# Kernel tuning notes

Hardware: AMD Instinct MI355X
Metric: run time of the kernel (lower is better)

## Reference

```python
import jax, jax.numpy as jnp
import numpy as np

HIDDEN_DIM = 128
ATTN_DIM = 64
B, N = 2, 512

def setup_inputs() -> dict:
    key = jax.random.key(0)
    ks = jax.random.split(key, 8)
    s = 0.05
    return {
        "X":    jax.random.normal(ks[0], (B, N, HIDDEN_DIM), dtype=jnp.float32),
        "Wo":   jax.random.normal(ks[1], (ATTN_DIM, HIDDEN_DIM), dtype=jnp.float32) * s,
        "W1":   jax.random.normal(ks[2], (ATTN_DIM, HIDDEN_DIM), dtype=jnp.float32) * s,
        "Wphi": jax.random.normal(ks[3], (ATTN_DIM,), dtype=jnp.float32) * s,
        "Wy":   jax.random.normal(ks[4], (HIDDEN_DIM, HIDDEN_DIM), dtype=jnp.float32) * s,
        "by":   jax.random.normal(ks[5], (HIDDEN_DIM,), dtype=jnp.float32) * s,
        "We":   jax.random.normal(ks[6], (HIDDEN_DIM, ATTN_DIM), dtype=jnp.float32) * s,
        "be":   jax.random.normal(ks[7], (HIDDEN_DIM,), dtype=jnp.float32) * s,
    }

def reference(X, Wo, W1, Wphi, Wy, by, We, be):
    # h_o, h_1: [B, N, A]
    h_o = jnp.einsum('bnc,ac->bna', X, Wo)
    h_1 = jnp.einsum('bnc,ac->bna', X, W1)
    # pairwise tanh edge features e_ij: [B, N, N, A]
    e = jnp.tanh(h_o[:, :, None, :] + h_1[:, None, :, :])
    # scores [B, N, N] via w_phi projection, row-wise softmax over j
    scores = jnp.einsum('bija,a->bij', e, Wphi)
    alpha = jax.nn.softmax(scores, axis=-1)
    # value path 1: Wy x_j -> aggregated by alpha (bmm)
    X_y = jnp.einsum('bnc,hc->bnh', X, Wy) + by
    part1 = jnp.einsum('bij,bjh->bih', alpha, X_y)
    # value path 2: We e_ij -> weighted sum over j
    eval_ = jnp.einsum('bija,ha->bijh', e, We) + be  # [B, N, N, H]
    part2 = jnp.einsum('bij,bijh->bih', alpha, eval_)
    return part1 + part2
```

## Files before the change

kernel.cpp:

```cpp
#include <hip/hip_runtime.h>

#define B_ 2
#define N_ 512
#define C_ 128
#define A_ 64
#define H_ 128

#define SC2L 2.885390081777927f
#define NEG2LE -2.885390081777927f

#define OFF_V   0
#define OFF_UT8 (OFF_V   + B_*N_*A_)
#define OFF_US8 (OFF_UT8 + B_*N_*A_/2)
#define OFF_XYP (OFF_US8 + B_*N_*A_/2)

#define WES_STRIDE 130

__device__ __forceinline__ float fexp2(float x) { return __builtin_amdgcn_exp2f(x); }
__device__ __forceinline__ float frcp(float x)  { return __builtin_amdgcn_rcpf(x); }
__device__ __forceinline__ unsigned f2bf(float x) {
  unsigned u = __float_as_uint(x);
  return (u + 0x7fffu + ((u >> 16) & 1u)) >> 16;
}
__device__ __forceinline__ float bf_lo(unsigned d) { return __uint_as_float(d << 16); }
__device__ __forceinline__ float bf_hi(unsigned d) { return __uint_as_float(d & 0xffff0000u); }

__global__ __launch_bounds__(256) void proj_kernel(
    const float* __restrict__ X, const float* __restrict__ by,
    const float* __restrict__ Wo, const float* __restrict__ W1,
    const float* __restrict__ Wy, float* __restrict__ ws) {
  __shared__ float xs[2*C_];
  int row0 = blockIdx.x * 2;
  int t = threadIdx.x;
  if (t < 2*C_) xs[t] = X[(size_t)row0*C_ + t];
  __syncthreads();

  const float* wrow;
  int col;
  if (t < 64)       { col = t;       wrow = Wo + (size_t)col*C_; }
  else if (t < 128) { col = t - 64;  wrow = W1 + (size_t)col*C_; }
  else              { col = t - 128; wrow = Wy + (size_t)col*C_; }

  const float4* w4 = (const float4*)wrow;
  float acc0 = 0.f, acc1 = 0.f;
  #pragma unroll 8
  for (int c4 = 0; c4 < C_/4; ++c4) {
    float4 w = w4[c4];
    int c = c4*4;
    acc0 = fmaf(xs[c+0], w.x, acc0);  acc1 = fmaf(xs[C_+c+0], w.x, acc1);
    acc0 = fmaf(xs[c+1], w.y, acc0);  acc1 = fmaf(xs[C_+c+1], w.y, acc1);
    acc0 = fmaf(xs[c+2], w.z, acc0);  acc1 = fmaf(xs[C_+c+2], w.z, acc1);
    acc0 = fmaf(xs[c+3], w.w, acc0);  acc1 = fmaf(xs[C_+c+3], w.w, acc1);
  }

  int b = row0 >> 9, n0 = row0 & (N_-1);

  if (t < 64) {
    float* o = ws + OFF_V + (size_t)row0*A_ + col;
    o[0] = fexp2(SC2L * acc0);
    o[A_] = fexp2(SC2L * acc1);
  } else if (t < 128) {
    int a = col;
    unsigned u0 = f2bf(fexp2(SC2L * acc0));
    unsigned u1 = f2bf(fexp2(SC2L * acc1));
    unsigned short* ut = (unsigned short*)(ws + OFF_UT8);
    size_t bA = ((size_t)(b*8 + (a >> 3))*N_ + n0)*8 + (a & 7);
    ut[bA] = (unsigned short)u0;
    ut[bA + 8] = (unsigned short)u1;
    unsigned short* us = (unsigned short*)(ws + OFF_US8);
    size_t bC = ((size_t)(b*64 + (n0 >> 3))*A_ + a)*8 + (n0 & 7);
    us[bC] = (unsigned short)u0;
    us[bC + 1] = (unsigned short)u1;
  } else {
    int h = col;
    float bb = by[h];
    unsigned xv0 = f2bf(acc0 + bb);
    unsigned xv1 = f2bf(acc1 + bb);
    unsigned* xp = (unsigned*)(ws + OFF_XYP);
    xp[(size_t)(b*(N_/2) + (n0 >> 1))*H_ + h] = xv0 | (xv1 << 16);
  }
}

__global__ __launch_bounds__(1024) void attn_kernel(
    const float* __restrict__ Wphi, const float* __restrict__ be,
    const float* __restrict__ We,
    const float* __restrict__ ws, float* __restrict__ out) {
  __shared__ __align__(16) float pkv[2][A_];
  __shared__ __align__(16) float pkw[A_];
  __shared__ float sc[2][N_];
  __shared__ float reds[16];
  __shared__ float ebw[2][16][A_];
  __shared__ float ebar[2][A_];
  __shared__ __align__(16) float p1s[2][32][H_];
  __shared__ float wes[A_*WES_STRIDE];

  int t = threadIdx.x;
  int w = t >> 6, lane = t & 63;
  int blk = blockIdx.x;
  int b = blk >> 8;
  int i0 = (blk & 255) * 2;
  int g0 = b*N_ + i0;

  const uint4* ut8 = (const uint4*)((const unsigned short*)(ws + OFF_UT8))
                     + (size_t)b*8*N_;
  const uint4* us8 = (const uint4*)((const unsigned short*)(ws + OFF_US8))
                     + (size_t)b*64*A_;
  const uint4* xy4 = (const uint4*)((const unsigned*)(ws + OFF_XYP))
                     + (size_t)b*(N_/2)*(H_/4);

  if (t < 2*A_) {
    int r = t >> 6, a = t & 63;
    pkv[r][a] = ws[OFF_V + (size_t)(g0 + r)*A_ + a];
  } else if (t < 3*A_) {
    pkw[t - 2*A_] = Wphi[t - 2*A_];
  }
  #pragma unroll
  for (int e = t; e < H_*A_; e += 1024) {
    int h = e >> 6, a = e & 63;
    wes[a*WES_STRIDE + h] = We[e];
  }
  __syncthreads();

  {
    int r = t >> 9, j = t & 511;
    const float4* pv4 = (const float4*)pkv[r];
    const float4* pw4 = (const float4*)pkw;
    float s = 0.f;
    #pragma unroll
    for (int g = 0; g < 8; ++g) {
      uint4 d = ut8[(size_t)g*N_ + j];
      float4 v0 = pv4[2*g], v1 = pv4[2*g + 1];
      float4 w0 = pw4[2*g], w1 = pw4[2*g + 1];
      s = fmaf(w0.x, frcp(fmaf(v0.x, bf_lo(d.x), 1.f)), s);
      s = fmaf(w0.y, frcp(fmaf(v0.y, bf_hi(d.x), 1.f)), s);
      s = fmaf(w0.z, frcp(fmaf(v0.z, bf_lo(d.y), 1.f)), s);
      s = fmaf(w0.w, frcp(fmaf(v0.w, bf_hi(d.y), 1.f)), s);
      s = fmaf(w1.x, frcp(fmaf(v1.x, bf_lo(d.z), 1.f)), s);
      s = fmaf(w1.y, frcp(fmaf(v1.y, bf_hi(d.z), 1.f)), s);
      s = fmaf(w1.z, frcp(fmaf(v1.z, bf_lo(d.w), 1.f)), s);
      s = fmaf(w1.w, frcp(fmaf(v1.w, bf_hi(d.w), 1.f)), s);
    }
    float p = fexp2(NEG2LE * s);
    sc[r][j] = p;
    float q = p;
    #pragma unroll
    for (int m = 1; m < 64; m <<= 1) q += __shfl_xor(q, m);
    if (lane == 0) reds[w] = q;
  }
  __syncthreads();

  {
    float v0 = pkv[0][lane], v1 = pkv[1][lane];
    const float4* s40 = (const float4*)sc[0];
    const float4* s41 = (const float4*)sc[1];
    float c0 = 0.f, c1 = 0.f;
    #pragma unroll
    for (int oo = 0; oo < 4; ++oo) {
      int o = oo*16 + w;
      uint4 d = us8[(size_t)o*A_ + lane];
      float u0 = bf_lo(d.x), u1 = bf_hi(d.x), u2 = bf_lo(d.y), u3 = bf_hi(d.y);
      float u4 = bf_lo(d.z), u5 = bf_hi(d.z), u6 = bf_lo(d.w), u7 = bf_hi(d.w);
      float4 pA0 = s40[o*2], pB0 = s40[o*2 + 1];
      float4 pA1 = s41[o*2], pB1 = s41[o*2 + 1];
      float r0 = frcp(fmaf(v0, u0, 1.f)), q0 = frcp(fmaf(v1, u0, 1.f));
      float r1 = frcp(fmaf(v0, u1, 1.f)), q1 = frcp(fmaf(v1, u1, 1.f));
      float r2 = frcp(fmaf(v0, u2, 1.f)), q2 = frcp(fmaf(v1, u2, 1.f));
      float r3 = frcp(fmaf(v0, u3, 1.f)), q3 = frcp(fmaf(v1, u3, 1.f));
      float r4 = frcp(fmaf(v0, u4, 1.f)), q4 = frcp(fmaf(v1, u4, 1.f));
      float r5 = frcp(fmaf(v0, u5, 1.f)), q5 = frcp(fmaf(v1, u5, 1.f));
      float r6 = frcp(fmaf(v0, u6, 1.f)), q6 = frcp(fmaf(v1, u6, 1.f));
      float r7 = frcp(fmaf(v0, u7, 1.f)), q7 = frcp(fmaf(v1, u7, 1.f));
      c0 = fmaf(pA0.x, r0, c0); c1 = fmaf(pA1.x, q0, c1);
      c0 = fmaf(pA0.y, r1, c0); c1 = fmaf(pA1.y, q1, c1);
      c0 = fmaf(pA0.z, r2, c0); c1 = fmaf(pA1.z, q2, c1);
      c0 = fmaf(pA0.w, r3, c0); c1 = fmaf(pA1.w, q3, c1);
      c0 = fmaf(pB0.x, r4, c0); c1 = fmaf(pB1.x, q4, c1);
      c0 = fmaf(pB0.y, r5, c0); c1 = fmaf(pB1.y, q5, c1);
      c0 = fmaf(pB0.z, r6, c0); c1 = fmaf(pB1.z, q6, c1);
      c0 = fmaf(pB0.w, r7, c0); c1 = fmaf(pB1.w, q7, c1);
    }
    ebw[0][w][lane] = c0;
    ebw[1][w][lane] = c1;
  }

  {
    int h4 = t & 31, qd = t >> 5;
    float d0 = 0.f, d1 = 0.f, d2 = 0.f, d3 = 0.f;
    float e0 = 0.f, e1 = 0.f, e2 = 0.f, e3 = 0.f;
    const float2* p20 = (const float2*)sc[0];
    const float2* p21 = (const float2*)sc[1];
    #pragma unroll
    for (int kc = 0; kc < 8; ++kc) {
      int k = qd*8 + kc;
      uint4 d = xy4[(size_t)k*(H_/4) + h4];
      float2 P0 = p20[k];
      float2 P1 = p21[k];
      float xa = bf_lo(d.x), xb = bf_hi(d.x);
      float xc = bf_lo(d.y), xd = bf_hi(d.y);
      float xe = bf_lo(d.z), xf = bf_hi(d.z);
      float xg = bf_lo(d.w), xh = bf_hi(d.w);
      d0 = fmaf(P0.x, xa, d0); d0 = fmaf(P0.y, xb, d0);
      d1 = fmaf(P0.x, xc, d1); d1 = fmaf(P0.y, xd, d1);
      d2 = fmaf(P0.x, xe, d2); d2 = fmaf(P0.y, xf, d2);
      d3 = fmaf(P0.x, xg, d3); d3 = fmaf(P0.y, xh, d3);
      e0 = fmaf(P1.x, xa, e0); e0 = fmaf(P1.y, xb, e0);
      e1 = fmaf(P1.x, xc, e1); e1 = fmaf(P1.y, xd, e1);
      e2 = fmaf(P1.x, xe, e2); e2 = fmaf(P1.y, xf, e2);
      e3 = fmaf(P1.x, xg, e3); e3 = fmaf(P1.y, xh, e3);
    }
    *(float4*)&p1s[0][qd][h4*4] = make_float4(d0, d1, d2, d3);
    *(float4*)&p1s[1][qd][h4*4] = make_float4(e0, e1, e2, e3);
  }
  __syncthreads();

  if (t < 2*A_) {
    int r = t >> 6, a = t & 63;
    float e = 0.f;
    #pragma unroll
    for (int k = 0; k < 16; ++k) e += ebw[r][k][a];
    float l = 0.f;
    #pragma unroll
    for (int k = 0; k < 8; ++k) l += reds[r*8 + k];
    ebar[r][a] = l - 2.0f*e;
  }
  __syncthreads();

  if (t < 2*H_) {
    int r = t >> 7, h = t & 127;
    float l = 0.f;
    #pragma unroll
    for (int k = 0; k < 8; ++k) l += reds[r*8 + k];
    float acc = 0.f;
    #pragma unroll
    for (int k = 0; k < 32; ++k) acc += p1s[r][k][h];
    float e2 = 0.f;
    #pragma unroll 8
    for (int a = 0; a < A_; ++a) e2 = fmaf(ebar[r][a], wes[a*WES_STRIDE + h], e2);
    out[(size_t)(g0 + r)*H_ + h] = (acc + e2) * frcp(l) + be[h];
  }
}

extern "C" void kernel_launch(void* const* d_in, const int* in_sizes, int n_in,
                              void* d_out, int out_size, void* d_ws, size_t ws_size,
                              hipStream_t stream) {
  const float* X    = (const float*)d_in[0];
  const float* Wo   = (const float*)d_in[1];
  const float* W1   = (const float*)d_in[2];
  const float* Wphi = (const float*)d_in[3];
  const float* Wy   = (const float*)d_in[4];
  const float* by   = (const float*)d_in[5];
  const float* We   = (const float*)d_in[6];
  const float* be   = (const float*)d_in[7];
  float* out = (float*)d_out;
  float* ws  = (float*)d_ws;

  hipLaunchKernelGGL(proj_kernel, dim3(B_*N_/2), dim3(256), 0, stream,
                     X, by, Wo, W1, Wy, ws);
  hipLaunchKernelGGL(attn_kernel, dim3(B_*N_/2), dim3(1024), 0, stream,
                     Wphi, be, We, ws, out);
}
```

Measured before the change: 92.50 us.

## Process four query rows per attention block to reuse key-side loads

Each attention block now handles four query rows instead of two, halving the grid to 256 blocks. Each key-side value loaded from global memory (ut8, us8, xy4) and the staged We matrix is reused across twice as many rows, which cuts global traffic and the per-block We staging cost. In exchange, register pressure and shared memory per block go up, and with fewer blocks the 256 CUs of the MI355X get only about one block each, lowering occupancy and latency hiding.

```diff
diff --git a/kernel.cpp b/kernel.cpp
--- a/kernel.cpp
+++ b/kernel.cpp
@@ -85,20 +85,20 @@
     const float* __restrict__ Wphi, const float* __restrict__ be,
     const float* __restrict__ We,
     const float* __restrict__ ws, float* __restrict__ out) {
-  __shared__ __align__(16) float pkv[2][A_];
+  __shared__ __align__(16) float pkv[4][A_];
   __shared__ __align__(16) float pkw[A_];
-  __shared__ float sc[2][N_];
-  __shared__ float reds[16];
-  __shared__ float ebw[2][16][A_];
-  __shared__ float ebar[2][A_];
-  __shared__ __align__(16) float p1s[2][32][H_];
+  __shared__ float sc[4][N_];
+  __shared__ float reds[4][8];
+  __shared__ float ebw[4][16][A_];
+  __shared__ float ebar[4][A_];
+  __shared__ __align__(16) float p1s[4][32][H_];
   __shared__ float wes[A_*WES_STRIDE];
 
   int t = threadIdx.x;
   int w = t >> 6, lane = t & 63;
   int blk = blockIdx.x;
-  int b = blk >> 8;
-  int i0 = (blk & 255) * 2;
+  int b = blk >> 7;
+  int i0 = (blk & 127) * 4;
   int g0 = b*N_ + i0;
 
   const uint4* ut8 = (const uint4*)((const unsigned short*)(ws + OFF_UT8))
@@ -108,11 +108,11 @@
   const uint4* xy4 = (const uint4*)((const unsigned*)(ws + OFF_XYP))
                      + (size_t)b*(N_/2)*(H_/4);
 
-  if (t < 2*A_) {
+  if (t < 4*A_) {
     int r = t >> 6, a = t & 63;
     pkv[r][a] = ws[OFF_V + (size_t)(g0 + r)*A_ + a];
-  } else if (t < 3*A_) {
-    pkw[t - 2*A_] = Wphi[t - 2*A_];
+  } else if (t < 5*A_) {
+    pkw[t - 4*A_] = Wphi[t - 4*A_];
   }
   #pragma unroll
   for (int e = t; e < H_*A_; e += 1024) {
@@ -122,38 +122,61 @@
   __syncthreads();
 
   {
-    int r = t >> 9, j = t & 511;
-    const float4* pv4 = (const float4*)pkv[r];
+    int r2 = t >> 9, j = t & 511;
+    const float4* pvA = (const float4*)pkv[r2];
+    const float4* pvB = (const float4*)pkv[r2 + 2];
     const float4* pw4 = (const float4*)pkw;
-    float s = 0.f;
+    float sA = 0.f, sB = 0.f;
     #pragma unroll
     for (int g = 0; g < 8; ++g) {
       uint4 d = ut8[(size_t)g*N_ + j];
-      float4 v0 = pv4[2*g], v1 = pv4[2*g + 1];
+      float4 a0 = pvA[2*g], a1 = pvA[2*g + 1];
+      float4 b0 = pvB[2*g], b1 = pvB[2*g + 1];
       float4 w0 = pw4[2*g], w1 = pw4[2*g + 1];
-      s = fmaf(w0.x, frcp(fmaf(v0.x, bf_lo(d.x), 1.f)), s);
-      s = fmaf(w0.y, frcp(fmaf(v0.y, bf_hi(d.x), 1.f)), s);
-      s = fmaf(w0.z, frcp(fmaf(v0.z, bf_lo(d.y), 1.f)), s);
-      s = fmaf(w0.w, frcp(fmaf(v0.w, bf_hi(d.y), 1.f)), s);
-      s = fmaf(w1.x, frcp(fmaf(v1.x, bf_lo(d.z), 1.f)), s);
-      s = fmaf(w1.y, frcp(fmaf(v1.y, bf_hi(d.z), 1.f)), s);
-      s = fmaf(w1.z, frcp(fmaf(v1.z, bf_lo(d.w), 1.f)), s);
-      s = fmaf(w1.w, frcp(fmaf(v1.w, bf_hi(d.w), 1.f)), s);
-    }
-    float p = fexp2(NEG2LE * s);
-    sc[r][j] = p;
-    float q = p;
-    #pragma unroll
-    for (int m = 1; m < 64; m <<= 1) q += __shfl_xor(q, m);
-    if (lane == 0) reds[w] = q;
+      float u0 = bf_lo(d.x), u1 = bf_hi(d.x), u2 = bf_lo(d.y), u3 = bf_hi(d.y);
+      float u4 = bf_lo(d.z), u5 = bf_hi(d.z), u6 = bf_lo(d.w), u7 = bf_hi(d.w);
+      sA = fmaf(w0.x, frcp(fmaf(a0.x, u0, 1.f)), sA);
+      sB = fmaf(w0.x, frcp(fmaf(b0.x, u0, 1.f)), sB);
+      sA = fmaf(w0.y, frcp(fmaf(a0.y, u1, 1.f)), sA);
+      sB = fmaf(w0.y, frcp(fmaf(b0.y, u1, 1.f)), sB);
+      sA = fmaf(w0.z, frcp(fmaf(a0.z, u2, 1.f)), sA);
+      sB = fmaf(w0.z, frcp(fmaf(b0.z, u2, 1.f)), sB);
+      sA = fmaf(w0.w, frcp(fmaf(a0.w, u3, 1.f)), sA);
+      sB = fmaf(w0.w, frcp(fmaf(b0.w, u3, 1.f)), sB);
+      sA = fmaf(w1.x, frcp(fmaf(a1.x, u4, 1.f)), sA);
+      sB = fmaf(w1.x, frcp(fmaf(b1.x, u4, 1.f)), sB);
+      sA = fmaf(w1.y, frcp(fmaf(a1.y, u5, 1.f)), sA);
+      sB = fmaf(w1.y, frcp(fmaf(b1.y, u5, 1.f)), sB);
+      sA = fmaf(w1.z, frcp(fmaf(a1.z, u6, 1.f)), sA);
+      sB = fmaf(w1.z, frcp(fmaf(b1.z, u6, 1.f)), sB);
+      sA = fmaf(w1.w, frcp(fmaf(a1.w, u7, 1.f)), sA);
+      sB = fmaf(w1.w, frcp(fmaf(b1.w, u7, 1.f)), sB);
+    }
+    float pA = fexp2(NEG2LE * sA);
+    float pB = fexp2(NEG2LE * sB);
+    sc[r2][j] = pA;
+    sc[r2 + 2][j] = pB;
+    float qA = pA, qB = pB;
+    #pragma unroll
+    for (int m = 1; m < 64; m <<= 1) {
+      qA += __shfl_xor(qA, m);
+      qB += __shfl_xor(qB, m);
+    }
+    if (lane == 0) {
+      reds[r2][w & 7] = qA;
+      reds[r2 + 2][w & 7] = qB;
+    }
   }
   __syncthreads();
 
   {
     float v0 = pkv[0][lane], v1 = pkv[1][lane];
+    float v2 = pkv[2][lane], v3 = pkv[3][lane];
     const float4* s40 = (const float4*)sc[0];
     const float4* s41 = (const float4*)sc[1];
-    float c0 = 0.f, c1 = 0.f;
+    const float4* s42 = (const float4*)sc[2];
+    const float4* s43 = (const float4*)sc[3];
+    float c0 = 0.f, c1 = 0.f, c2 = 0.f, c3 = 0.f;
     #pragma unroll
     for (int oo = 0; oo < 4; ++oo) {
       int o = oo*16 + w;
@@ -162,74 +185,93 @@
       float u4 = bf_lo(d.z), u5 = bf_hi(d.z), u6 = bf_lo(d.w), u7 = bf_hi(d.w);
       float4 pA0 = s40[o*2], pB0 = s40[o*2 + 1];
       float4 pA1 = s41[o*2], pB1 = s41[o*2 + 1];
-      float r0 = frcp(fmaf(v0, u0, 1.f)), q0 = frcp(fmaf(v1, u0, 1.f));
-      float r1 = frcp(fmaf(v0, u1, 1.f)), q1 = frcp(fmaf(v1, u1, 1.f));
-      float r2 = frcp(fmaf(v0, u2, 1.f)), q2 = frcp(fmaf(v1, u2, 1.f));
-      float r3 = frcp(fmaf(v0, u3, 1.f)), q3 = frcp(fmaf(v1, u3, 1.f));
-      float r4 = frcp(fmaf(v0, u4, 1.f)), q4 = frcp(fmaf(v1, u4, 1.f));
-      float r5 = frcp(fmaf(v0, u5, 1.f)), q5 = frcp(fmaf(v1, u5, 1.f));
-      float r6 = frcp(fmaf(v0, u6, 1.f)), q6 = frcp(fmaf(v1, u6, 1.f));
-      float r7 = frcp(fmaf(v0, u7, 1.f)), q7 = frcp(fmaf(v1, u7, 1.f));
-      c0 = fmaf(pA0.x, r0, c0); c1 = fmaf(pA1.x, q0, c1);
-      c0 = fmaf(pA0.y, r1, c0); c1 = fmaf(pA1.y, q1, c1);
-      c0 = fmaf(pA0.z, r2, c0); c1 = fmaf(pA1.z, q2, c1);
-      c0 = fmaf(pA0.w, r3, c0); c1 = fmaf(pA1.w, q3, c1);
-      c0 = fmaf(pB0.x, r4, c0); c1 = fmaf(pB1.x, q4, c1);
-      c0 = fmaf(pB0.y, r5, c0); c1 = fmaf(pB1.y, q5, c1);
-      c0 = fmaf(pB0.z, r6, c0); c1 = fmaf(pB1.z, q6, c1);
-      c0 = fmaf(pB0.w, r7, c0); c1 = fmaf(pB1.w, q7, c1);
+      float4 pA2 = s42[o*2], pB2 = s42[o*2 + 1];
+      float4 pA3 = s43[o*2], pB3 = s43[o*2 + 1];
+      #define PC_STEP(UU, F) { \
+        float r0 = frcp(fmaf(v0, UU, 1.f)); \
+        float r1 = frcp(fmaf(v1, UU, 1.f)); \
+        float r2v = frcp(fmaf(v2, UU, 1.f)); \
+        float r3v = frcp(fmaf(v3, UU, 1.f)); \
+        c0 = fmaf(pA0.F, r0, c0); c1 = fmaf(pA1.F, r1, c1); \
+        c2 = fmaf(pA2.F, r2v, c2); c3 = fmaf(pA3.F, r3v, c3); }
+      #define PC_STEP2(UU, F) { \
+        float r0 = frcp(fmaf(v0, UU, 1.f)); \
+        float r1 = frcp(fmaf(v1, UU, 1.f)); \
+        float r2v = frcp(fmaf(v2, UU, 1.f)); \
+        float r3v = frcp(fmaf(v3, UU, 1.f)); \
+        c0 = fmaf(pB0.F, r0, c0); c1 = fmaf(pB1.F, r1, c1); \
+        c2 = fmaf(pB2.F, r2v, c2); c3 = fmaf(pB3.F, r3v, c3); }
+      PC_STEP(u0, x) PC_STEP(u1, y) PC_STEP(u2, z) PC_STEP(u3, w)
+      PC_STEP2(u4, x) PC_STEP2(u5, y) PC_STEP2(u6, z) PC_STEP2(u7, w)
+      #undef PC_STEP
+      #undef PC_STEP2
     }
     ebw[0][w][lane] = c0;
     ebw[1][w][lane] = c1;
+    ebw[2][w][lane] = c2;
+    ebw[3][w][lane] = c3;
   }
 
   {
     int h4 = t & 31, qd = t >> 5;
-    float d0 = 0.f, d1 = 0.f, d2 = 0.f, d3 = 0.f;
-    float e0 = 0.f, e1 = 0.f, e2 = 0.f, e3 = 0.f;
+    float s00=0.f,s01=0.f,s02=0.f,s03=0.f;
+    float s10=0.f,s11=0.f,s12=0.f,s13=0.f;
+    float s20=0.f,s21=0.f,s22=0.f,s23=0.f;
+    float s30=0.f,s31=0.f,s32=0.f,s33=0.f;
     const float2* p20 = (const float2*)sc[0];
     const float2* p21 = (const float2*)sc[1];
+    const float2* p22 = (const float2*)sc[2];
+    const float2* p23 = (const float2*)sc[3];
     #pragma unroll
     for (int kc = 0; kc < 8; ++kc) {
       int k = qd*8 + kc;
       uint4 d = xy4[(size_t)k*(H_/4) + h4];
-      float2 P0 = p20[k];
-      float2 P1 = p21[k];
+      float2 P0 = p20[k], P1 = p21[k], P2 = p22[k], P3 = p23[k];
       float xa = bf_lo(d.x), xb = bf_hi(d.x);
       float xc = bf_lo(d.y), xd = bf_hi(d.y);
       float xe = bf_lo(d.z), xf = bf_hi(d.z);
       float xg = bf_lo(d.w), xh = bf_hi(d.w);
-      d0 = fmaf(P0.x, xa, d0); d0 = fmaf(P0.y, xb, d0);
-      d1 = fmaf(P0.x, xc, d1); d1 = fmaf(P0.y, xd, d1);
-      d2 = fmaf(P0.x, xe, d2); d2 = fmaf(P0.y, xf, d2);
-      d3 = fmaf(P0.x, xg, d3); d3 = fmaf(P0.y, xh, d3);
-      e0 = fmaf(P1.x, xa, e0); e0 = fmaf(P1.y, xb, e0);
-      e1 = fmaf(P1.x, xc, e1); e1 = fmaf(P1.y, xd, e1);
-      e2 = fmaf(P1.x, xe, e2); e2 = fmaf(P1.y, xf, e2);
-      e3 = fmaf(P1.x, xg, e3); e3 = fmaf(P1.y, xh, e3);
-    }
-    *(float4*)&p1s[0][qd][h4*4] = make_float4(d0, d1, d2, d3);
-    *(float4*)&p1s[1][qd][h4*4] = make_float4(e0, e1, e2, e3);
-  }
-  __syncthreads();
-
-  if (t < 2*A_) {
+      s00 = fmaf(P0.x, xa, s00); s00 = fmaf(P0.y, xb, s00);
+      s01 = fmaf(P0.x, xc, s01); s01 = fmaf(P0.y, xd, s01);
+      s02 = fmaf(P0.x, xe, s02); s02 = fmaf(P0.y, xf, s02);
+      s03 = fmaf(P0.x, xg, s03); s03 = fmaf(P0.y, xh, s03);
+      s10 = fmaf(P1.x, xa, s10); s10 = fmaf(P1.y, xb, s10);
+      s11 = fmaf(P1.x, xc, s11); s11 = fmaf(P1.y, xd, s11);
+      s12 = fmaf(P1.x, xe, s12); s12 = fmaf(P1.y, xf, s12);
+      s13 = fmaf(P1.x, xg, s13); s13 = fmaf(P1.y, xh, s13);
+      s20 = fmaf(P2.x, xa, s20); s20 = fmaf(P2.y, xb, s20);
+      s21 = fmaf(P2.x, xc, s21); s21 = fmaf(P2.y, xd, s21);
+      s22 = fmaf(P2.x, xe, s22); s22 = fmaf(P2.y, xf, s22);
+      s23 = fmaf(P2.x, xg, s23); s23 = fmaf(P2.y, xh, s23);
+      s30 = fmaf(P3.x, xa, s30); s30 = fmaf(P3.y, xb, s30);
+      s31 = fmaf(P3.x, xc, s31); s31 = fmaf(P3.y, xd, s31);
+      s32 = fmaf(P3.x, xe, s32); s32 = fmaf(P3.y, xf, s32);
+      s33 = fmaf(P3.x, xg, s33); s33 = fmaf(P3.y, xh, s33);
+    }
+    *(float4*)&p1s[0][qd][h4*4] = make_float4(s00, s01, s02, s03);
+    *(float4*)&p1s[1][qd][h4*4] = make_float4(s10, s11, s12, s13);
+    *(float4*)&p1s[2][qd][h4*4] = make_float4(s20, s21, s22, s23);
+    *(float4*)&p1s[3][qd][h4*4] = make_float4(s30, s31, s32, s33);
+  }
+  __syncthreads();
+
+  if (t < 4*A_) {
     int r = t >> 6, a = t & 63;
     float e = 0.f;
     #pragma unroll
     for (int k = 0; k < 16; ++k) e += ebw[r][k][a];
     float l = 0.f;
     #pragma unroll
-    for (int k = 0; k < 8; ++k) l += reds[r*8 + k];
+    for (int k = 0; k < 8; ++k) l += reds[r][k];
     ebar[r][a] = l - 2.0f*e;
   }
   __syncthreads();
 
-  if (t < 2*H_) {
+  if (t < 4*H_) {
     int r = t >> 7, h = t & 127;
     float l = 0.f;
     #pragma unroll
-    for (int k = 0; k < 8; ++k) l += reds[r*8 + k];
+    for (int k = 0; k < 8; ++k) l += reds[r][k];
     float acc = 0.f;
     #pragma unroll
     for (int k = 0; k < 32; ++k) acc += p1s[r][k][h];
@@ -256,6 +298,6 @@
 
   hipLaunchKernelGGL(proj_kernel, dim3(B_*N_/2), dim3(256), 0, stream,
                      X, by, Wo, W1, Wy, ws);
-  hipLaunchKernelGGL(attn_kernel, dim3(B_*N_/2), dim3(1024), 0, stream,
+  hipLaunchKernelGGL(attn_kernel, dim3(B_*N_/4), dim3(1024), 0, stream,
                      Wphi, be, We, ws, out);
 }
```

Result: faster. 90.38 us (-2.3%).
